# Optimization experiments

Hardware: AMD Instinct MI355X
Metric: run time of the kernel (lower is better)

Reference implementation:

```python
import jax, jax.numpy as jnp
import numpy as np

B, TASK, LQ, D = 16, 80, 1024, 768
HH, HD, P, NL = 12, 64, 4, 1
HF, WF = 64, 64
LIN = HF * WF
EPS = 1e-6


def _ln(x, w, b):
    mu = jnp.mean(x, -1, keepdims=True)
    var = jnp.mean(jnp.square(x - mu), -1, keepdims=True)
    return (x - mu) * jax.lax.rsqrt(var + EPS) * w + b


def _bilinear(value_l, loc_l, Hl, Wl):
    # value_l: [B, HH, S, HD]; loc_l: [B, LQ, HH, P, 2] in [0,1]
    # replicates F.grid_sample(align_corners=False, padding_mode='zeros')
    b, hh, s, hd = value_l.shape
    lq, p = loc_l.shape[1], loc_l.shape[3]
    x = loc_l[..., 0] * Wl - 0.5
    y = loc_l[..., 1] * Hl - 0.5
    x0 = jnp.floor(x)
    y0 = jnp.floor(y)
    out = jnp.zeros((b, hh, lq, p, hd), value_l.dtype)
    for dx in (0, 1):
        for dy in (0, 1):
            xc = x0 + dx
            yc = y0 + dy
            w = (1.0 - jnp.abs(x - xc)) * (1.0 - jnp.abs(y - yc))
            valid = (xc >= 0) & (xc <= Wl - 1) & (yc >= 0) & (yc <= Hl - 1)
            w = jnp.where(valid, w, 0.0)
            xi = jnp.clip(xc, 0, Wl - 1).astype(jnp.int32)
            yi = jnp.clip(yc, 0, Hl - 1).astype(jnp.int32)
            lin = (yi * Wl + xi).transpose(0, 2, 1, 3).reshape(b, hh, lq * p, 1)
            v = jnp.take_along_axis(value_l, lin, axis=2).reshape(b, hh, lq, p, hd)
            out = out + v * w.transpose(0, 2, 1, 3)[..., None]
    return out


def _forward(query, reference_points, feat, spatial_shapes, level_start_index,
             qn_w, qn_b, fn_w, fn_b, gamma,
             W_off, b_off, W_attw, b_attw, W_val, b_val, W_out, b_out):
    ss = np.asarray(spatial_shapes)
    lsi = np.asarray(level_start_index)
    tt = query[:, :TASK]
    q = query[:, TASK:]
    bq, lq, _ = q.shape
    qn = _ln(q, qn_w, qn_b)
    fn = _ln(feat, fn_w, fn_b)
    # value projection: [B, Lin, D] -> [B, HH, Lin, HD]
    value = (fn @ W_val + b_val).reshape(bq, -1, HH, HD).transpose(0, 2, 1, 3)
    off = (qn @ W_off + b_off).reshape(bq, lq, HH, NL, P, 2)
    aw = (qn @ W_attw + b_attw).reshape(bq, lq, HH, NL * P)
    aw = jax.nn.softmax(aw, axis=-1).reshape(bq, lq, HH, NL, P)
    # offset normalizer is [W, H] per level
    norm = jnp.stack([ss[:, 1].astype(jnp.float32), ss[:, 0].astype(jnp.float32)], -1)
    loc = reference_points[:, :, None, :, None, :] + off / norm[None, None, None, :, None, :]
    out = jnp.zeros((bq, lq, HH, HD), query.dtype)
    for l in range(ss.shape[0]):
        Hl, Wl = int(ss[l, 0]), int(ss[l, 1])
        st = int(lsi[l])
        vl = value[:, :, st:st + Hl * Wl]
        sampled = _bilinear(vl, loc[:, :, :, l], Hl, Wl)  # [B,HH,LQ,P,HD]
        out = out + jnp.einsum('bhqpd,bqhp->bqhd', sampled, aw[:, :, :, l])
    attn = out.reshape(bq, lq, HH * HD) @ W_out + b_out
    q = q + gamma * attn
    return jnp.concatenate([tt, q], axis=1)


def setup_inputs():
    key = jax.random.key(0)
    ks = jax.random.split(key, 10)
    s = 0.02
    return {
        "query": jax.random.normal(ks[0], (B, TASK + LQ, D), jnp.float32),
        "reference_points": jax.random.uniform(ks[1], (B, LQ, NL, 2), dtype=jnp.float32),
        "feat": jax.random.normal(ks[2], (B, LIN, D), jnp.float32),
        "spatial_shapes": jnp.array([[HF, WF]], jnp.int32),
        "level_start_index": jnp.array([0], jnp.int32),
        "qn_w": jnp.ones((D,), jnp.float32),
        "qn_b": jnp.zeros((D,), jnp.float32),
        "fn_w": jnp.ones((D,), jnp.float32),
        "fn_b": jnp.zeros((D,), jnp.float32),
        "gamma": 0.1 * jax.random.normal(ks[3], (D,), jnp.float32),
        "W_off": s * jax.random.normal(ks[4], (D, HH * NL * P * 2), jnp.float32),
        "b_off": s * jax.random.normal(ks[5], (HH * NL * P * 2,), jnp.float32),
        "W_attw": s * jax.random.normal(ks[6], (D, HH * NL * P), jnp.float32),
        "b_attw": s * jax.random.normal(ks[7], (HH * NL * P,), jnp.float32),
        "W_val": s * jax.random.normal(ks[8], (D, D), jnp.float32),
        "b_val": jnp.zeros((D,), jnp.float32),
        "W_out": s * jax.random.normal(ks[9], (D, D), jnp.float32),
        "b_out": jnp.zeros((D,), jnp.float32),
    }


def reference(query, reference_points, feat, spatial_shapes, level_start_index, qn_w, qn_b, fn_w, fn_b, gamma, W_off, b_off, W_attw, b_attw, W_val, b_val, W_out, b_out):
    return _forward(query, reference_points, feat, spatial_shapes, level_start_index,
                    qn_w, qn_b, fn_w, fn_b, gamma,
                    W_off, b_off, W_attw, b_attw, W_val, b_val, W_out, b_out)
```

## Files before the change

### kernel.cpp

```cpp
#include <hip/hip_runtime.h>
#include <hip/hip_bf16.h>

using bf16 = __hip_bfloat16;
typedef __attribute__((ext_vector_type(8))) short short8;
typedef __attribute__((ext_vector_type(4))) short short4v;
typedef __attribute__((ext_vector_type(4))) float floatx4;
typedef __attribute__((ext_vector_type(2))) float floatx2;

#define B_    16
#define TASK_ 80
#define LQ_   1024
#define D_    768
#define HH_   12
#define HD_   64
#define LIN_  4096
#define MQ_   (B_*LQ_)
#define MF_   (B_*LIN_)
#define QR_   (TASK_+LQ_)

static constexpr size_t OFF_VAL  = 0;
static constexpr size_t OFF_FN   = OFF_VAL + (size_t)MF_*D_*2;
static constexpr size_t OFF_QN   = OFF_FN  + (size_t)MF_*D_*2;
static constexpr size_t OFF_PREP = OFF_QN  + (size_t)MQ_*D_*2;
static constexpr size_t OFF_WVT  = OFF_PREP + (size_t)MQ_*HH_*64;
static constexpr size_t OFF_WOT  = OFF_WVT + (size_t)D_*D_*2;
static constexpr size_t OFF_WCT  = OFF_WOT + (size_t)D_*D_*2;

__device__ __forceinline__ void async16(const void* g, void* l) {
  __builtin_amdgcn_global_load_lds((const __attribute__((address_space(1))) void*)g,
                                   (__attribute__((address_space(3))) void*)l, 16, 0, 0);
}

__global__ __launch_bounds__(256) void k_wln(const float* __restrict__ Wv, const float* __restrict__ Wo,
                                             const float* __restrict__ Woff, const float* __restrict__ Wat,
                                             bf16* __restrict__ WvT, bf16* __restrict__ WoT,
                                             bf16* __restrict__ WcT,
                                             const float* __restrict__ query, const float* __restrict__ feat,
                                             const float* __restrict__ qw, const float* __restrict__ qb,
                                             const float* __restrict__ fw, const float* __restrict__ fb,
                                             bf16* __restrict__ qn, bf16* __restrict__ fn) {
  __shared__ float t[64][65];
  int bid = blockIdx.x;
  if (bid < 288) {
    const float* W = (bid < 144) ? Wv : Wo;
    bf16* WT = (bid < 144) ? WvT : WoT;
    int lb = (bid < 144) ? bid : bid - 144;
    int bx = lb % 12, by = lb / 12;
    int n0 = bx*64, k0 = by*64;
    int col = threadIdx.x & 63, rg = threadIdx.x >> 6;
    #pragma unroll
    for (int i=0;i<16;++i) { int row = i*4+rg; t[row][col] = W[(size_t)(k0+row)*D_ + n0+col]; }
    __syncthreads();
    #pragma unroll
    for (int i=0;i<16;++i) { int row = i*4+rg; WT[(size_t)(n0+row)*D_ + k0+col] = __float2bfloat16(t[col][row]); }
    return;
  }
  if (bid < 1056) {
    int idx = (bid-288)*256 + threadIdx.x;
    int j = idx / D_, k = idx - j*D_;
    float v = 0.f;
    if (j < 96)       v = Woff[(size_t)k*96 + j];
    else if (j < 144) v = Wat[(size_t)k*48 + (j-96)];
    WcT[idx] = __float2bfloat16(v);
    return;
  }
  int r = (bid-1056)*4 + (threadIdx.x>>6);
  int lane = threadIdx.x & 63;
  const float* src; const float* w; const float* bia; bf16* dst;
  if (r < MQ_) {
    int bat = r >> 10, rr = r & 1023;
    src = query + ((size_t)bat*QR_ + TASK_ + rr)*D_;
    w = qw; bia = qb; dst = qn + (size_t)r*D_;
  } else {
    int fr = r - MQ_;
    src = feat + (size_t)fr*D_;
    w = fw; bia = fb; dst = fn + (size_t)fr*D_;
  }
  float4 v[3], ww[3], bb[3];
  #pragma unroll
  for (int j=0;j<3;++j) v[j]  = ((const float4*)src)[lane + 64*j];
  #pragma unroll
  for (int j=0;j<3;++j) ww[j] = ((const float4*)w)[lane + 64*j];
  #pragma unroll
  for (int j=0;j<3;++j) bb[j] = ((const float4*)bia)[lane + 64*j];
  float s = 0.f, s2 = 0.f;
  #pragma unroll
  for (int j=0;j<3;++j) {
    s  += v[j].x + v[j].y + v[j].z + v[j].w;
    s2 += v[j].x*v[j].x + v[j].y*v[j].y + v[j].z*v[j].z + v[j].w*v[j].w;
  }
  #pragma unroll
  for (int o=32;o>0;o>>=1){ s += __shfl_xor(s,o); s2 += __shfl_xor(s2,o); }
  float mu  = s*(1.f/D_);
  float var = s2*(1.f/D_) - mu*mu;
  float rstd = rsqrtf(var + 1e-6f);
  #pragma unroll
  for (int j=0;j<3;++j) {
    short4v o4;
    o4[0] = (short)__bfloat16_as_ushort(__float2bfloat16((v[j].x-mu)*rstd*ww[j].x + bb[j].x));
    o4[1] = (short)__bfloat16_as_ushort(__float2bfloat16((v[j].y-mu)*rstd*ww[j].y + bb[j].y));
    o4[2] = (short)__bfloat16_as_ushort(__float2bfloat16((v[j].z-mu)*rstd*ww[j].z + bb[j].z));
    o4[3] = (short)__bfloat16_as_ushort(__float2bfloat16((v[j].w-mu)*rstd*ww[j].w + bb[j].w));
    *(short4v*)(dst + 4*(lane + 64*j)) = o4;
  }
}

__global__ __launch_bounds__(256) void k_offprep(const bf16* __restrict__ A, const bf16* __restrict__ BT,
                                                 const float* __restrict__ b_off, const float* __restrict__ b_attw,
                                                 const float* __restrict__ refp, char* __restrict__ prepc,
                                                 const float* __restrict__ query, float* __restrict__ out) {
  __shared__ char lds[49152];
  const int tid = threadIdx.x, wid = tid>>6, lane = tid&63;
  const int bm = blockIdx.x*64;
  const int K = D_;
  const int srow = tid>>2;
  const int skb = ((tid&3) ^ ((tid>>3)&3))*8;
  const bf16* gA  = A  + (size_t)(bm + srow)*K + skb;
  const bf16* gB  = BT + (size_t)srow*K + skb;
  const int dstbase = wid<<10;
  const int rb = (lane&15)*64 + ((((lane>>4) ^ ((lane>>1)&3)))<<4);
  floatx4 acc[4][3] = {};
  auto stage = [&](int k0, char* buf) {
    async16(gA + k0,                 buf + dstbase);
    async16(gB + k0,                 buf + 4096  + dstbase);
    async16(gB + (size_t)64*K + k0,  buf + 8192  + dstbase);
    async16(gB + (size_t)128*K + k0, buf + 12288 + dstbase);
  };
  stage(0,  lds);
  stage(32, lds + 16384);
  const int NT = K >> 5;
  int cur = 0, nxt = 2;
  for (int k = 0; k < NT; ++k) {
    if (k < NT-1) asm volatile("s_waitcnt vmcnt(4)" ::: "memory");
    else          asm volatile("s_waitcnt vmcnt(0)" ::: "memory");
    __builtin_amdgcn_s_barrier();
    __builtin_amdgcn_sched_barrier(0);
    if (k + 2 < NT) stage((k+2)*32, lds + nxt*16384);
    const char* ldsA = lds + cur*16384; const char* ldsB = ldsA + 4096;
    short8 af[4], bf[3];
    #pragma unroll
    for (int i=0;i<4;++i) af[i] = *(const short8*)(ldsA + (i*16)*64 + rb);
    #pragma unroll
    for (int j=0;j<3;++j) bf[j] = *(const short8*)(ldsB + (wid*48 + j*16)*64 + rb);
    #pragma unroll
    for (int mi=0;mi<4;++mi)
      #pragma unroll
      for (int ni=0;ni<3;++ni)
        acc[mi][ni] = __builtin_amdgcn_mfma_f32_16x16x32_bf16(af[mi], bf[ni], acc[mi][ni], 0, 0, 0);
    cur = (cur==2) ? 0 : cur+1;
    nxt = (nxt==2) ? 0 : nxt+1;
  }
  __syncthreads();
  float* oa = (float*)lds;
  const int rowb = (lane>>4)*4, col = lane&15;
  #pragma unroll
  for (int mi=0;mi<4;++mi) {
    #pragma unroll
    for (int ni=0;ni<3;++ni) {
      const int gn = wid*48 + ni*16 + col;
      if (gn < 144) {
        const float bv = (gn < 96) ? b_off[gn] : b_attw[gn-96];
        #pragma unroll
        for (int r=0;r<4;++r) {
          const int rl = mi*16 + rowb + r;
          oa[rl*148 + gn] = acc[mi][ni][r] + bv;
        }
      }
    }
  }
  __syncthreads();
  #pragma unroll
  for (int i=0;i<12;++i) {
    int item = tid + i*256;
    int rl = item / 48;
    int hp = item - rl*48;
    int h = hp >> 2, p = hp & 3;
    int m = bm + rl;
    const float* row = oa + rl*148;
    float l0 = row[96+h*4+0], l1 = row[96+h*4+1], l2 = row[96+h*4+2], l3 = row[96+h*4+3];
    float mx = fmaxf(fmaxf(l0,l1), fmaxf(l2,l3));
    float e0 = expf(l0-mx), e1 = expf(l1-mx), e2 = expf(l2-mx), e3 = expf(l3-mx);
    float inv = 1.f/(e0+e1+e2+e3);
    float ep = (p==0)?e0:(p==1)?e1:(p==2)?e2:e3;
    float awp = ep*inv;
    float x = refp[(size_t)m*2+0]*64.f - 0.5f + row[h*8+p*2+0];
    float y = refp[(size_t)m*2+1]*64.f - 0.5f + row[h*8+p*2+1];
    float x0f = floorf(x), y0f = floorf(y);
    int ix = (int)x0f, iy = (int)y0f;
    float fx = x-x0f, fy = y-y0f;
    float wx[2] = {1.f-fx, fx}, wy[2] = {1.f-fy, fy};
    short4v wq, pq;
    #pragma unroll
    for (int c=0;c<4;++c) {
      int dx = c&1, dy = c>>1;
      int xc = ix+dx, yc = iy+dy;
      bool valid = ((unsigned)xc < 64u) && ((unsigned)yc < 64u);
      float w = valid ? awp*wx[dx]*wy[dy] : 0.f;
      int xi = min(max(xc,0),63), yi = min(max(yc,0),63);
      wq[c] = (short)__bfloat16_as_ushort(__float2bfloat16(w));
      pq[c] = (short)(yi*64+xi);
    }
    char* gb = prepc + ((size_t)(m*HH_ + h))*64;
    *(short4v*)(gb + p*8)      = wq;
    *(short4v*)(gb + 32 + p*8) = pq;
  }
  #pragma unroll
  for (int i=0;i<4;++i) {
    int ci = blockIdx.x*256 + tid + i*65536;
    if (ci < B_*TASK_*D_/4) {
      const int perb = TASK_*D_/4;
      int b = ci / perb, r = ci - b*perb;
      const float4* s = (const float4*)(query + (size_t)b*QR_*D_) + r;
      float4* dd = (float4*)(out + (size_t)b*QR_*D_) + r;
      *dd = *s;
    }
  }
}

template<int MODE>
__global__ __launch_bounds__(512, 2) void k_gemm256(const bf16* __restrict__ A, const bf16* __restrict__ BT,
                                                    const float* __restrict__ bias0, void* __restrict__ outp,
                                                    const float* __restrict__ query, const float* __restrict__ gamma) {
  __shared__ char lds[98304];
  const int K = D_;
  const int tid = threadIdx.x, wid = tid>>6, lane = tid&63;
  const int nwg = gridDim.x*gridDim.y;
  const int d = blockIdx.y*gridDim.x + blockIdx.x;
  const int logical = (d & 7)*(nwg>>3) + (d>>3);
  const int bm = (logical/3)*256, bn = (logical%3)*256;
  const int wm = wid>>2, wn = wid&3;
  const int srow = tid>>2;
  const int sslot = ((tid&3) ^ ((tid>>3)&3))*8;
  const bf16* gA0 = A  + (size_t)(bm + srow)*K + sslot;
  const bf16* gA1 = A  + (size_t)(bm + 128 + srow)*K + sslot;
  const bf16* gB0 = BT + (size_t)(bn + srow)*K + sslot;
  const bf16* gB1 = BT + (size_t)(bn + 128 + srow)*K + sslot;
  const int dstbase = (tid>>6)<<10;
  const int rb = (lane&15)*64 + ((((lane>>4) ^ ((lane>>1)&3)))<<4);
  floatx4 acc[8][4] = {};
  auto stageAll = [&](int k0, char* buf) {
    async16(gA0+k0, buf + dstbase);
    async16(gA1+k0, buf + 8192 + dstbase);
    async16(gB0+k0, buf + 16384 + dstbase);
    async16(gB1+k0, buf + 24576 + dstbase);
  };
  stageAll(0,  lds);
  stageAll(32, lds + 32768);
  const int NT = K >> 5;
  int cur = 0, nxt = 2;
  for (int k = 0; k < NT; ++k) {
    if (k < NT-1) asm volatile("s_waitcnt vmcnt(4)" ::: "memory");
    else          asm volatile("s_waitcnt vmcnt(0)" ::: "memory");
    __builtin_amdgcn_s_barrier();
    __builtin_amdgcn_sched_barrier(0);
    const int kk = (k+2)*32;
    const bool pf = (k+2 < NT);
    const char* lA = lds + cur*32768;
    const char* lB = lA + 16384;
    char* bufn = lds + nxt*32768;
    short8 af[8], bfr[4];
    if (pf) async16(gA0+kk, bufn + dstbase);
    #pragma unroll
    for (int i=0;i<4;++i) af[i] = *(const short8*)(lA + (wm*128 + i*16)*64 + rb);
    #pragma unroll
    for (int i=0;i<2;++i) bfr[i] = *(const short8*)(lB + (wn*64 + i*16)*64 + rb);
    __builtin_amdgcn_s_barrier();
    __builtin_amdgcn_s_setprio(1);
    #pragma unroll
    for (int mi=0;mi<4;++mi)
      #pragma unroll
      for (int ni=0;ni<2;++ni)
        acc[mi][ni] = __builtin_amdgcn_mfma_f32_16x16x32_bf16(af[mi], bfr[ni], acc[mi][ni], 0, 0, 0);
    __builtin_amdgcn_s_setprio(0);
    __builtin_amdgcn_s_barrier();
    __builtin_amdgcn_sched_barrier(0);
    if (pf) async16(gA1+kk, bufn + 8192 + dstbase);
    #pragma unroll
    for (int i=2;i<4;++i) bfr[i] = *(const short8*)(lB + (wn*64 + i*16)*64 + rb);
    __builtin_amdgcn_s_barrier();
    __builtin_amdgcn_s_setprio(1);
    #pragma unroll
    for (int mi=0;mi<4;++mi)
      #pragma unroll
      for (int ni=2;ni<4;++ni)
        acc[mi][ni] = __builtin_amdgcn_mfma_f32_16x16x32_bf16(af[mi], bfr[ni], acc[mi][ni], 0, 0, 0);
    __builtin_amdgcn_s_setprio(0);
    __builtin_amdgcn_s_barrier();
    __builtin_amdgcn_sched_barrier(0);
    if (pf) async16(gB0+kk, bufn + 16384 + dstbase);
    #pragma unroll
    for (int i=4;i<8;++i) af[i] = *(const short8*)(lA + (wm*128 + i*16)*64 + rb);
    __builtin_amdgcn_s_barrier();
    __builtin_amdgcn_s_setprio(1);
    #pragma unroll
    for (int mi=4;mi<8;++mi)
      #pragma unroll
      for (int ni=0;ni<2;++ni)
        acc[mi][ni] = __builtin_amdgcn_mfma_f32_16x16x32_bf16(af[mi], bfr[ni], acc[mi][ni], 0, 0, 0);
    __builtin_amdgcn_s_setprio(0);
    __builtin_amdgcn_s_barrier();
    __builtin_amdgcn_sched_barrier(0);
    if (pf) async16(gB1+kk, bufn + 24576 + dstbase);
    __builtin_amdgcn_s_barrier();
    __builtin_amdgcn_s_setprio(1);
    #pragma unroll
    for (int mi=4;mi<8;++mi)
      #pragma unroll
      for (int ni=2;ni<4;++ni)
        acc[mi][ni] = __builtin_amdgcn_mfma_f32_16x16x32_bf16(af[mi], bfr[ni], acc[mi][ni], 0, 0, 0);
    __builtin_amdgcn_s_setprio(0);
    __builtin_amdgcn_sched_barrier(0);
    cur = (cur==2) ? 0 : cur+1;
    nxt = (nxt==2) ? 0 : nxt+1;
  }
  const int rowb = (lane>>4)*4, col = lane&15;
  #pragma unroll
  for (int mi=0;mi<8;++mi) {
    #pragma unroll
    for (int ni=0;ni<4;++ni) {
      const int gn = bn + wn*64 + ni*16 + col;
      const float bv = bias0[gn];
      #pragma unroll
      for (int r=0;r<4;++r) {
        const int gm = bm + wm*128 + mi*16 + rowb + r;
        if constexpr (MODE==0) {
          const int h = gn >> 6, hd = gn & 63;
          const int b = gm >> 12, pix = gm & 4095;
          float v = acc[mi][ni][r] + bv;
          unsigned char f8 = (unsigned char)(__builtin_amdgcn_cvt_pk_fp8_f32(v, v, 0, false) & 0xff);
          ((unsigned char*)outp)[(((size_t)(b*HH_+h)*LIN_ + pix)<<6) + hd] = f8;
        } else {
          const int bq = gm >> 10, lq = gm & 1023;
          size_t idx = ((size_t)bq*QR_ + TASK_ + lq)*D_ + gn;
          ((float*)outp)[idx] = query[idx] + gamma[gn]*(acc[mi][ni][r] + bv);
        }
      }
    }
  }
}

__global__ __launch_bounds__(256) void k_sample(const char* __restrict__ prepc,
                                                const unsigned char* __restrict__ value,
                                                bf16* __restrict__ sampout) {
  int g  = blockIdx.x*8 + (threadIdx.x>>5);
  int l  = threadIdx.x & 31;
  int c8 = l >> 2, p = l & 3;
  int h = g % HH_, m = g / HH_;
  int b = m >> 10;
  const char* gb = prepc + (size_t)g*64;
  short4v wq = *(const short4v*)(gb + p*8);
  short4v pq = *(const short4v*)(gb + 32 + p*8);
  const unsigned char* vb = value + (((size_t)(b*HH_+h))<<18) + (c8<<3);
  float a[8] = {};
  #pragma unroll
  for (int c=0;c<4;++c) {
    float w = __uint_as_float(((unsigned)(unsigned short)wq[c])<<16);
    int pix = (int)(unsigned short)pq[c];
    uint2 d = *(const uint2*)(vb + ((size_t)pix<<6));
    floatx2 f0 = __builtin_amdgcn_cvt_pk_f32_fp8(d.x, false);
    floatx2 f1 = __builtin_amdgcn_cvt_pk_f32_fp8(d.x, true);
    floatx2 f2 = __builtin_amdgcn_cvt_pk_f32_fp8(d.y, false);
    floatx2 f3 = __builtin_amdgcn_cvt_pk_f32_fp8(d.y, true);
    a[0] += w*f0.x; a[1] += w*f0.y;
    a[2] += w*f1.x; a[3] += w*f1.y;
    a[4] += w*f2.x; a[5] += w*f2.y;
    a[6] += w*f3.x; a[7] += w*f3.y;
  }
  #pragma unroll
  for (int j=0;j<8;++j) { a[j] += __shfl_xor(a[j],1); a[j] += __shfl_xor(a[j],2); }
  if (p == 0) {
    short8 o;
    #pragma unroll
    for (int j=0;j<8;++j)
      o[j] = (short)__bfloat16_as_ushort(__float2bfloat16(a[j]));
    *(short8*)(sampout + (size_t)m*D_ + h*64 + c8*8) = o;
  }
}

extern "C" void kernel_launch(void* const* d_in, const int* in_sizes, int n_in,
                              void* d_out, int out_size, void* d_ws, size_t ws_size,
                              hipStream_t stream) {
  (void)in_sizes; (void)n_in; (void)out_size; (void)ws_size;
  const float* query = (const float*)d_in[0];
  const float* refp  = (const float*)d_in[1];
  const float* feat  = (const float*)d_in[2];
  const float* qn_w  = (const float*)d_in[5];
  const float* qn_b  = (const float*)d_in[6];
  const float* fn_w  = (const float*)d_in[7];
  const float* fn_b  = (const float*)d_in[8];
  const float* gamma = (const float*)d_in[9];
  const float* W_off = (const float*)d_in[10];
  const float* b_off = (const float*)d_in[11];
  const float* W_attw= (const float*)d_in[12];
  const float* b_attw= (const float*)d_in[13];
  const float* W_val = (const float*)d_in[14];
  const float* b_val = (const float*)d_in[15];
  const float* W_out = (const float*)d_in[16];
  const float* b_out = (const float*)d_in[17];
  char*  ws  = (char*)d_ws;
  float* out = (float*)d_out;

  unsigned char* wsVal = (unsigned char*)(ws + OFF_VAL);
  bf16* wsFn   = (bf16*)(ws + OFF_FN);
  bf16* wsQn   = (bf16*)(ws + OFF_QN);
  char* wsPrep = ws + OFF_PREP;
  bf16* wsWvT  = (bf16*)(ws + OFF_WVT);
  bf16* wsWoT  = (bf16*)(ws + OFF_WOT);
  bf16* wsWcT  = (bf16*)(ws + OFF_WCT);
  bf16* wsSamp = wsFn;

  k_wln<<<1056 + (MQ_+MF_)/4, 256, 0, stream>>>(W_val, W_out, W_off, W_attw, wsWvT, wsWoT, wsWcT,
                                                query, feat, qn_w, qn_b, fn_w, fn_b, wsQn, wsFn);
  k_offprep<<<MQ_/64, 256, 0, stream>>>(wsQn, wsWcT, b_off, b_attw, refp, wsPrep, query, out);
  k_gemm256<0><<<dim3(MF_/256, 3), 512, 0, stream>>>(wsFn, wsWvT, b_val, wsVal, nullptr, nullptr);
  k_sample<<<(MQ_*HH_)/8, 256, 0, stream>>>(wsPrep, wsVal, wsSamp);
  k_gemm256<2><<<dim3(MQ_/256, 3), 512, 0, stream>>>(wsSamp, wsWoT, b_out, out, query, gamma);
}
```

Before: 251.6 us.

## Run value projection GEMM in FP8 with FP8 LayerNorm output and weights

The feature LayerNorm now writes FP8 instead of bf16, the value weight transpose is stored as FP8, and a new FP8 MFMA GEMM kernel replaces the bf16 value projection. Halving operand bytes cuts memory traffic for the largest GEMM (65536x768x768) and uses the faster FP8 matrix instructions. It loads through LDS with 4-byte async copies and a triple-buffered pipeline. The cost is lower input precision for the value path, which raises numerical error.

```diff
diff --git a/kernel.cpp b/kernel.cpp
--- a/kernel.cpp
+++ b/kernel.cpp
@@ -30,20 +30,26 @@
   __builtin_amdgcn_global_load_lds((const __attribute__((address_space(1))) void*)g,
                                    (__attribute__((address_space(3))) void*)l, 16, 0, 0);
 }
+__device__ __forceinline__ void async4(const void* g, void* l) {
+  __builtin_amdgcn_global_load_lds((const __attribute__((address_space(1))) void*)g,
+                                   (__attribute__((address_space(3))) void*)l, 4, 0, 0);
+}
+__device__ __forceinline__ unsigned char to_fp8(float v) {
+  return (unsigned char)(__builtin_amdgcn_cvt_pk_fp8_f32(v, v, 0, false) & 0xff);
+}
 
 __global__ __launch_bounds__(256) void k_wln(const float* __restrict__ Wv, const float* __restrict__ Wo,
                                              const float* __restrict__ Woff, const float* __restrict__ Wat,
-                                             bf16* __restrict__ WvT, bf16* __restrict__ WoT,
+                                             unsigned char* __restrict__ WvT8, bf16* __restrict__ WoT,
                                              bf16* __restrict__ WcT,
                                              const float* __restrict__ query, const float* __restrict__ feat,
                                              const float* __restrict__ qw, const float* __restrict__ qb,
                                              const float* __restrict__ fw, const float* __restrict__ fb,
-                                             bf16* __restrict__ qn, bf16* __restrict__ fn) {
+                                             bf16* __restrict__ qn, unsigned char* __restrict__ fn8) {
   __shared__ float t[64][65];
   int bid = blockIdx.x;
   if (bid < 288) {
     const float* W = (bid < 144) ? Wv : Wo;
-    bf16* WT = (bid < 144) ? WvT : WoT;
     int lb = (bid < 144) ? bid : bid - 144;
     int bx = lb % 12, by = lb / 12;
     int n0 = bx*64, k0 = by*64;
@@ -51,8 +57,13 @@
     #pragma unroll
     for (int i=0;i<16;++i) { int row = i*4+rg; t[row][col] = W[(size_t)(k0+row)*D_ + n0+col]; }
     __syncthreads();
-    #pragma unroll
-    for (int i=0;i<16;++i) { int row = i*4+rg; WT[(size_t)(n0+row)*D_ + k0+col] = __float2bfloat16(t[col][row]); }
+    if (bid < 144) {
+      #pragma unroll
+      for (int i=0;i<16;++i) { int row = i*4+rg; WvT8[(size_t)(n0+row)*D_ + k0+col] = to_fp8(t[col][row]); }
+    } else {
+      #pragma unroll
+      for (int i=0;i<16;++i) { int row = i*4+rg; WoT[(size_t)(n0+row)*D_ + k0+col] = __float2bfloat16(t[col][row]); }
+    }
     return;
   }
   if (bid < 1056) {
@@ -66,15 +77,17 @@
   }
   int r = (bid-1056)*4 + (threadIdx.x>>6);
   int lane = threadIdx.x & 63;
-  const float* src; const float* w; const float* bia; bf16* dst;
-  if (r < MQ_) {
+  const bool isQ = (r < MQ_);
+  const float* src; const float* w; const float* bia;
+  bf16* dstq = nullptr; unsigned char* dstf = nullptr;
+  if (isQ) {
     int bat = r >> 10, rr = r & 1023;
     src = query + ((size_t)bat*QR_ + TASK_ + rr)*D_;
-    w = qw; bia = qb; dst = qn + (size_t)r*D_;
+    w = qw; bia = qb; dstq = qn + (size_t)r*D_;
   } else {
     int fr = r - MQ_;
     src = feat + (size_t)fr*D_;
-    w = fw; bia = fb; dst = fn + (size_t)fr*D_;
+    w = fw; bia = fb; dstf = fn8 + (size_t)fr*D_;
   }
   float4 v[3], ww[3], bb[3];
   #pragma unroll
@@ -96,12 +109,22 @@
   float rstd = rsqrtf(var + 1e-6f);
   #pragma unroll
   for (int j=0;j<3;++j) {
-    short4v o4;
-    o4[0] = (short)__bfloat16_as_ushort(__float2bfloat16((v[j].x-mu)*rstd*ww[j].x + bb[j].x));
-    o4[1] = (short)__bfloat16_as_ushort(__float2bfloat16((v[j].y-mu)*rstd*ww[j].y + bb[j].y));
-    o4[2] = (short)__bfloat16_as_ushort(__float2bfloat16((v[j].z-mu)*rstd*ww[j].z + bb[j].z));
-    o4[3] = (short)__bfloat16_as_ushort(__float2bfloat16((v[j].w-mu)*rstd*ww[j].w + bb[j].w));
-    *(short4v*)(dst + 4*(lane + 64*j)) = o4;
+    float r0 = (v[j].x-mu)*rstd*ww[j].x + bb[j].x;
+    float r1 = (v[j].y-mu)*rstd*ww[j].y + bb[j].y;
+    float r2 = (v[j].z-mu)*rstd*ww[j].z + bb[j].z;
+    float r3 = (v[j].w-mu)*rstd*ww[j].w + bb[j].w;
+    if (isQ) {
+      short4v o4;
+      o4[0] = (short)__bfloat16_as_ushort(__float2bfloat16(r0));
+      o4[1] = (short)__bfloat16_as_ushort(__float2bfloat16(r1));
+      o4[2] = (short)__bfloat16_as_ushort(__float2bfloat16(r2));
+      o4[3] = (short)__bfloat16_as_ushort(__float2bfloat16(r3));
+      *(short4v*)(dstq + 4*(lane + 64*j)) = o4;
+    } else {
+      unsigned lo = (unsigned)__builtin_amdgcn_cvt_pk_fp8_f32(r0, r1, 0, false);
+      unsigned pk = (unsigned)__builtin_amdgcn_cvt_pk_fp8_f32(r2, r3, (int)lo, true);
+      *(unsigned*)(dstf + 4*(lane + 64*j)) = pk;
+    }
   }
 }
 
@@ -213,6 +236,122 @@
       const float4* s = (const float4*)(query + (size_t)b*QR_*D_) + r;
       float4* dd = (float4*)(out + (size_t)b*QR_*D_) + r;
       *dd = *s;
+    }
+  }
+}
+
+__global__ __launch_bounds__(512, 2) void k_gemm_fp8(const unsigned char* __restrict__ A,
+                                                     const unsigned char* __restrict__ BT,
+                                                     const float* __restrict__ bias0,
+                                                     unsigned char* __restrict__ outp) {
+  __shared__ char lds[49152];
+  const int tid = threadIdx.x, wid = tid>>6, lane = tid&63;
+  const int nwg = gridDim.x*gridDim.y;
+  const int d = blockIdx.y*gridDim.x + blockIdx.x;
+  const int logical = (d & 7)*(nwg>>3) + (d>>3);
+  const int bm = (logical/3)*256, bn = (logical%3)*256;
+  const int wm = wid>>2, wn = wid&3;
+  int srcAoff[4], srcBoff[4];
+  #pragma unroll
+  for (int i=0;i<4;++i) {
+    int g = wid*64 + lane + i*512;
+    int row = g >> 3, sp = (g>>1)&3, half = g&1;
+    int s = sp ^ ((row>>2)&3);
+    srcAoff[i] = (bm + row)*D_ + s*8 + half*4;
+    srcBoff[i] = (bn + row)*D_ + s*8 + half*4;
+  }
+  const int dstb = wid*256;
+  const int rx = (lane&15)*32 + ((((lane>>4) ^ ((lane>>2)&3)))<<3);
+  floatx4 acc[8][4] = {};
+  auto stageAll = [&](int k0, char* buf) {
+    #pragma unroll
+    for (int i=0;i<4;++i) async4(A + srcAoff[i] + k0, buf + i*2048 + dstb);
+    #pragma unroll
+    for (int i=0;i<4;++i) async4(BT + srcBoff[i] + k0, buf + 8192 + i*2048 + dstb);
+  };
+  stageAll(0,  lds);
+  stageAll(32, lds + 16384);
+  const int NT = D_ >> 5;
+  int cur = 0, nxt = 2;
+  for (int k = 0; k < NT; ++k) {
+    if (k < NT-1) asm volatile("s_waitcnt vmcnt(8)" ::: "memory");
+    else          asm volatile("s_waitcnt vmcnt(0)" ::: "memory");
+    __builtin_amdgcn_s_barrier();
+    __builtin_amdgcn_sched_barrier(0);
+    const int kk = (k+2)*32;
+    const bool pf = (k+2 < NT);
+    const char* lA = lds + cur*16384;
+    const char* lB = lA + 8192;
+    char* bufn = lds + nxt*16384;
+    long af[8], bfr[4];
+    if (pf) { async4(A+srcAoff[0]+kk, bufn + dstb); async4(A+srcAoff[1]+kk, bufn + 2048 + dstb); }
+    #pragma unroll
+    for (int i=0;i<4;++i) af[i] = *(const long*)(lA + (wm*128 + i*16)*32 + rx);
+    #pragma unroll
+    for (int i=0;i<2;++i) bfr[i] = *(const long*)(lB + (wn*64 + i*16)*32 + rx);
+    __builtin_amdgcn_s_barrier();
+    __builtin_amdgcn_s_setprio(1);
+    #pragma unroll
+    for (int mi=0;mi<4;++mi)
+      #pragma unroll
+      for (int ni=0;ni<2;++ni)
+        acc[mi][ni] = __builtin_amdgcn_mfma_f32_16x16x32_fp8_fp8(af[mi], bfr[ni], acc[mi][ni], 0, 0, 0);
+    __builtin_amdgcn_s_setprio(0);
+    __builtin_amdgcn_s_barrier();
+    __builtin_amdgcn_sched_barrier(0);
+    if (pf) { async4(A+srcAoff[2]+kk, bufn + 4096 + dstb); async4(A+srcAoff[3]+kk, bufn + 6144 + dstb); }
+    #pragma unroll
+    for (int i=2;i<4;++i) bfr[i] = *(const long*)(lB + (wn*64 + i*16)*32 + rx);
+    __builtin_amdgcn_s_barrier();
+    __builtin_amdgcn_s_setprio(1);
+    #pragma unroll
+    for (int mi=0;mi<4;++mi)
+      #pragma unroll
+      for (int ni=2;ni<4;++ni)
+        acc[mi][ni] = __builtin_amdgcn_mfma_f32_16x16x32_fp8_fp8(af[mi], bfr[ni], acc[mi][ni], 0, 0, 0);
+    __builtin_amdgcn_s_setprio(0);
+    __builtin_amdgcn_s_barrier();
+    __builtin_amdgcn_sched_barrier(0);
+    if (pf) { async4(BT+srcBoff[0]+kk, bufn + 8192 + dstb); async4(BT+srcBoff[1]+kk, bufn + 10240 + dstb); }
+    #pragma unroll
+    for (int i=4;i<8;++i) af[i] = *(const long*)(lA + (wm*128 + i*16)*32 + rx);
+    __builtin_amdgcn_s_barrier();
+    __builtin_amdgcn_s_setprio(1);
+    #pragma unroll
+    for (int mi=4;mi<8;++mi)
+      #pragma unroll
+      for (int ni=0;ni<2;++ni)
+        acc[mi][ni] = __builtin_amdgcn_mfma_f32_16x16x32_fp8_fp8(af[mi], bfr[ni], acc[mi][ni], 0, 0, 0);
+    __builtin_amdgcn_s_setprio(0);
+    __builtin_amdgcn_s_barrier();
+    __builtin_amdgcn_sched_barrier(0);
+    if (pf) { async4(BT+srcBoff[2]+kk, bufn + 12288 + dstb); async4(BT+srcBoff[3]+kk, bufn + 14336 + dstb); }
+    __builtin_amdgcn_s_barrier();
+    __builtin_amdgcn_s_setprio(1);
+    #pragma unroll
+    for (int mi=4;mi<8;++mi)
+      #pragma unroll
+      for (int ni=2;ni<4;++ni)
+        acc[mi][ni] = __builtin_amdgcn_mfma_f32_16x16x32_fp8_fp8(af[mi], bfr[ni], acc[mi][ni], 0, 0, 0);
+    __builtin_amdgcn_s_setprio(0);
+    __builtin_amdgcn_sched_barrier(0);
+    cur = (cur==2) ? 0 : cur+1;
+    nxt = (nxt==2) ? 0 : nxt+1;
+  }
+  const int rowb = (lane>>4)*4, col = lane&15;
+  #pragma unroll
+  for (int mi=0;mi<8;++mi) {
+    #pragma unroll
+    for (int ni=0;ni<4;++ni) {
+      const int gn = bn + wn*64 + ni*16 + col;
+      const float bv = bias0[gn];
+      const int h = gn >> 6, hd = gn & 63;
+      #pragma unroll
+      for (int r=0;r<4;++r) {
+        const int gm = bm + wm*128 + mi*16 + rowb + r;
+        const int b = gm >> 12, pix = gm & 4095;
+        outp[(((size_t)(b*HH_+h)*LIN_ + pix)<<6) + hd] = to_fp8(acc[mi][ni][r] + bv);
+      }
     }
   }
 }
@@ -323,17 +462,9 @@
       #pragma unroll
       for (int r=0;r<4;++r) {
         const int gm = bm + wm*128 + mi*16 + rowb + r;
-        if constexpr (MODE==0) {
-          const int h = gn >> 6, hd = gn & 63;
-          const int b = gm >> 12, pix = gm & 4095;
-          float v = acc[mi][ni][r] + bv;
-          unsigned char f8 = (unsigned char)(__builtin_amdgcn_cvt_pk_fp8_f32(v, v, 0, false) & 0xff);
-          ((unsigned char*)outp)[(((size_t)(b*HH_+h)*LIN_ + pix)<<6) + hd] = f8;
-        } else {
-          const int bq = gm >> 10, lq = gm & 1023;
-          size_t idx = ((size_t)bq*QR_ + TASK_ + lq)*D_ + gn;
-          ((float*)outp)[idx] = query[idx] + gamma[gn]*(acc[mi][ni][r] + bv);
-        }
+        const int bq = gm >> 10, lq = gm & 1023;
+        size_t idx = ((size_t)bq*QR_ + TASK_ + lq)*D_ + gn;
+        ((float*)outp)[idx] = query[idx] + gamma[gn]*(acc[mi][ni][r] + bv);
       }
     }
   }
@@ -401,18 +532,18 @@
   float* out = (float*)d_out;
 
   unsigned char* wsVal = (unsigned char*)(ws + OFF_VAL);
-  bf16* wsFn   = (bf16*)(ws + OFF_FN);
+  unsigned char* wsFn8 = (unsigned char*)(ws + OFF_FN);
   bf16* wsQn   = (bf16*)(ws + OFF_QN);
   char* wsPrep = ws + OFF_PREP;
-  bf16* wsWvT  = (bf16*)(ws + OFF_WVT);
+  unsigned char* wsWvT8 = (unsigned char*)(ws + OFF_WVT);
   bf16* wsWoT  = (bf16*)(ws + OFF_WOT);
   bf16* wsWcT  = (bf16*)(ws + OFF_WCT);
-  bf16* wsSamp = wsFn;
-
-  k_wln<<<1056 + (MQ_+MF_)/4, 256, 0, stream>>>(W_val, W_out, W_off, W_attw, wsWvT, wsWoT, wsWcT,
-                                                query, feat, qn_w, qn_b, fn_w, fn_b, wsQn, wsFn);
+  bf16* wsSamp = (bf16*)(ws + OFF_FN);
+
+  k_wln<<<1056 + (MQ_+MF_)/4, 256, 0, stream>>>(W_val, W_out, W_off, W_attw, wsWvT8, wsWoT, wsWcT,
+                                                query, feat, qn_w, qn_b, fn_w, fn_b, wsQn, wsFn8);
   k_offprep<<<MQ_/64, 256, 0, stream>>>(wsQn, wsWcT, b_off, b_attw, refp, wsPrep, query, out);
-  k_gemm256<0><<<dim3(MF_/256, 3), 512, 0, stream>>>(wsFn, wsWvT, b_val, wsVal, nullptr, nullptr);
+  k_gemm_fp8<<<dim3(MF_/256, 3), 512, 0, stream>>>(wsFn8, wsWvT8, b_val, wsVal);
   k_sample<<<(MQ_*HH_)/8, 256, 0, stream>>>(wsPrep, wsVal, wsSamp);
   k_gemm256<2><<<dim3(MQ_/256, 3), 512, 0, stream>>>(wsSamp, wsWoT, b_out, out, query, gamma);
 }
```

Result: faster. 242.3 us (median of 2 runs) (-3.7%).
